# Kernel optimization log

Hardware: AMD Instinct MI355X
Metric: run time of the kernel (lower is better)

The kernel has to match this reference:

```python
import jax, jax.numpy as jnp
import numpy as np

B, T, I, H, S = 4096, 512, 4, 32, 4


def setup_inputs() -> dict:
    key = jax.random.key(0)
    ks = jax.random.split(key, 8)
    sc_ih = 1.0 / np.sqrt(H)
    return {
        "x": jax.random.normal(ks[0], (B, T, I), dtype=jnp.float32),
        "h0": jnp.zeros((1, B, H), dtype=jnp.float32),
        # PyTorch GRU params: weight_ih_l0 [3H, I] (r,z,n order), weight_hh_l0 [3H, H], biases [3H]
        "w_ih": jax.random.uniform(ks[1], (3 * H, I), jnp.float32, -sc_ih, sc_ih),
        "w_hh": jax.random.uniform(ks[2], (3 * H, H), jnp.float32, -sc_ih, sc_ih),
        "b_ih": jax.random.uniform(ks[3], (3 * H,), jnp.float32, -sc_ih, sc_ih),
        "b_hh": jax.random.uniform(ks[4], (3 * H,), jnp.float32, -sc_ih, sc_ih),
        "w_proj": jax.random.uniform(ks[5], (S, H), jnp.float32, -sc_ih, sc_ih),
        "b_proj": jax.random.uniform(ks[6], (S,), jnp.float32, -sc_ih, sc_ih),
    }


def _gru(x, h0, w_ih, w_hh, b_ih, b_hh):
    # Precompute input contributions for all timesteps: [B, T, 3H]
    xg = jnp.einsum('bti,gi->btg', x, w_ih) + b_ih
    xg_t = jnp.transpose(xg, (1, 0, 2))  # [T, B, 3H]
    h = h0[0]  # [B, H] (num_layers == 1)
    Hdim = w_hh.shape[1]

    def step(h, xg_step):
        hg = h @ w_hh.T + b_hh  # [B, 3H]
        xr, xz, xn = jnp.split(xg_step, 3, axis=-1)
        hr, hz, hn = jnp.split(hg, 3, axis=-1)
        r = jax.nn.sigmoid(xr + hr)
        z = jax.nn.sigmoid(xz + hz)
        n = jnp.tanh(xn + r * hn)
        h_new = (1.0 - z) * n + z * h
        return h_new, h_new

    hT, outs = jax.lax.scan(step, h, xg_t)
    out = jnp.transpose(outs, (1, 0, 2))  # [B, T, H]
    return out, hT[None]  # hn: [1, B, H]


def reference(x, h0, w_ih, w_hh, b_ih, b_hh, w_proj, b_proj):
    out, hn = _gru(x, h0, w_ih, w_hh, b_ih, b_hh)
    state = jnp.einsum('bth,sh->bts', out, w_proj) + b_proj  # [B, T, S]
    return state, hn
```

## Files before the change

### kernel.cpp

```cpp
#include <hip/hip_runtime.h>
#include <stdint.h>

#define BB 4096
#define TT 512
#define II 4
#define HH 32
#define SS 4

__device__ __forceinline__ float fast_sigm(float a) {
  return __builtin_amdgcn_rcpf(1.0f + __expf(-a));
}
__device__ __forceinline__ float fast_tanh(float y) {
  return 1.0f - 2.0f * __builtin_amdgcn_rcpf(__expf(2.0f * y) + 1.0f);
}

__global__ __launch_bounds__(256, 2) void gru_kernel(
    const float* __restrict__ x, const float* __restrict__ h0,
    const float* __restrict__ w_ih, const float* __restrict__ w_hh,
    const float* __restrict__ b_ih, const float* __restrict__ b_hh,
    const float* __restrict__ w_proj, const float* __restrict__ b_proj,
    float* __restrict__ out) {
  const int tid  = threadIdx.x;
  const int wid  = tid >> 6;
  const int lane = tid & 63;
  const int g    = lane >> 5;
  const int j    = lane & 31;
  const int row  = wid * 2 + g;
  const int b    = blockIdx.x * 8 + row;

  __shared__ float lds_h[8][36];
  float* lrow = &lds_h[row][0];

  const float4* whh4 = (const float4*)w_hh;
  float4 wr[8], wz[8], wn[8];
#pragma unroll
  for (int c = 0; c < 8; ++c) {
    wr[c] = whh4[(0 * HH + j) * 8 + c];
    wz[c] = whh4[(1 * HH + j) * 8 + c];
    wn[c] = whh4[(2 * HH + j) * 8 + c];
  }
  const float4* wih4 = (const float4*)w_ih;
  const float4 wir = wih4[0 * HH + j];
  const float4 wiz = wih4[1 * HH + j];
  const float4 win = wih4[2 * HH + j];
  const float bir = b_ih[0 * HH + j], biz = b_ih[1 * HH + j], bin_ = b_ih[2 * HH + j];
  const float bhr = b_hh[0 * HH + j], bhz = b_hh[1 * HH + j], bhn = b_hh[2 * HH + j];

  const int s_idx = j & 3;
  const int c_idx = j >> 2;
  const float4* wp4 = (const float4*)w_proj;
  const float4 wp = wp4[s_idx * 8 + c_idx];
  const float bp = b_proj[s_idx];

  float h_self = h0[(size_t)b * HH + j];
  lrow[j] = h_self;

  const float4* xp = (const float4*)(x + (size_t)b * TT * II);
  float* outp = out + (size_t)b * TT * SS;

  float4 xv = xp[0];

  for (int t = 0; t < TT; ++t) {
    float4 xvn = xp[(t + 1 < TT) ? (t + 1) : t];

    float4 ha[8];
#pragma unroll
    for (int c = 0; c < 8; ++c) ha[c] = *(const float4*)&lrow[c * 4];

    float xr = fmaf(wir.x, xv.x, fmaf(wir.y, xv.y, fmaf(wir.z, xv.z, fmaf(wir.w, xv.w, bir))));
    float xz = fmaf(wiz.x, xv.x, fmaf(wiz.y, xv.y, fmaf(wiz.z, xv.z, fmaf(wiz.w, xv.w, biz))));
    float xn = fmaf(win.x, xv.x, fmaf(win.y, xv.y, fmaf(win.z, xv.z, fmaf(win.w, xv.w, bin_))));

    float hr = bhr, hz = bhz, hn = bhn;
#pragma unroll
    for (int c = 0; c < 8; ++c) {
      hr = fmaf(wr[c].x, ha[c].x, hr); hr = fmaf(wr[c].y, ha[c].y, hr);
      hr = fmaf(wr[c].z, ha[c].z, hr); hr = fmaf(wr[c].w, ha[c].w, hr);
      hz = fmaf(wz[c].x, ha[c].x, hz); hz = fmaf(wz[c].y, ha[c].y, hz);
      hz = fmaf(wz[c].z, ha[c].z, hz); hz = fmaf(wz[c].w, ha[c].w, hz);
      hn = fmaf(wn[c].x, ha[c].x, hn); hn = fmaf(wn[c].y, ha[c].y, hn);
      hn = fmaf(wn[c].z, ha[c].z, hn); hn = fmaf(wn[c].w, ha[c].w, hn);
    }

    const float r  = fast_sigm(xr + hr);
    const float zz = fast_sigm(xz + hz);
    const float nn = fast_tanh(fmaf(r, hn, xn));
    const float hnew = fmaf(zz, h_self - nn, nn);
    h_self = hnew;

    lrow[j] = hnew;

    const float4 hc = *(const float4*)&lrow[c_idx * 4];
    float v = fmaf(wp.x, hc.x, fmaf(wp.y, hc.y, fmaf(wp.z, hc.z, wp.w * hc.w)));
    v += __shfl_xor(v, 4, 64);
    v += __shfl_xor(v, 8, 64);
    v += __shfl_xor(v, 16, 64);
    if (c_idx == 0) {
      outp[t * SS + s_idx] = v + bp;
    }

    xv = xvn;
  }

  out[(size_t)BB * TT * SS + (size_t)b * HH + j] = h_self;
}

extern "C" void kernel_launch(void* const* d_in, const int* in_sizes, int n_in,
                              void* d_out, int out_size, void* d_ws, size_t ws_size,
                              hipStream_t stream) {
  const float* x      = (const float*)d_in[0];
  const float* h0     = (const float*)d_in[1];
  const float* w_ih   = (const float*)d_in[2];
  const float* w_hh   = (const float*)d_in[3];
  const float* b_ih   = (const float*)d_in[4];
  const float* b_hh   = (const float*)d_in[5];
  const float* w_proj = (const float*)d_in[6];
  const float* b_proj = (const float*)d_in[7];
  float* out = (float*)d_out;

  dim3 grid(BB / 8), block(256);
  hipLaunchKernelGGL(gru_kernel, grid, block, 0, stream,
                     x, h0, w_ih, w_hh, b_ih, b_hh, w_proj, b_proj, out);
}
```

Measured before the change: 332.5 us.

## Split gate work across half-waves with packed fp16 weights and mixed FMA

Restructures the per-step GRU work so each half-wave computes two gate projections for both batch rows of the wave. Group 0 does r and z, and group 1 does n plus the output projection, which is folded in as an extra weight row. Partial sums are exchanged with a 32-lane shuffle. Weights are packed to fp16 in registers and used via v_fma_mix_f32, halving weight register count and removing the separate projection reduction shuffles. The projection is delayed by one step, which adds an extra loop iteration, and fp16 weights reduce accuracy.

```diff
diff --git a/kernel.cpp b/kernel.cpp
--- a/kernel.cpp
+++ b/kernel.cpp
@@ -3,7 +3,6 @@
 
 #define BB 4096
 #define TT 512
-#define II 4
 #define HH 32
 #define SS 4
 
@@ -14,95 +13,121 @@
   return 1.0f - 2.0f * __builtin_amdgcn_rcpf(__expf(2.0f * y) + 1.0f);
 }
 
-__global__ __launch_bounds__(256, 2) void gru_kernel(
-    const float* __restrict__ x, const float* __restrict__ h0,
-    const float* __restrict__ w_ih, const float* __restrict__ w_hh,
-    const float* __restrict__ b_ih, const float* __restrict__ b_hh,
-    const float* __restrict__ w_proj, const float* __restrict__ b_proj,
-    float* __restrict__ out) {
+#define PKH(dst, lo, hi)                                                       \
+  asm volatile("v_cvt_pkrtz_f16_f32 %0, %1, %2" : "=v"(dst) : "v"(lo), "v"(hi))
+#define MIXLO(acc, w, h)                                                       \
+  asm("v_fma_mix_f32 %0, %1, %2, %0 op_sel:[0,0,0] op_sel_hi:[1,0,0]"          \
+      : "+v"(acc) : "v"(w), "v"(h))
+#define MIXHI(acc, w, h)                                                       \
+  asm("v_fma_mix_f32 %0, %1, %2, %0 op_sel:[1,0,0] op_sel_hi:[1,0,0]"          \
+      : "+v"(acc) : "v"(w), "v"(h))
+#define MIXQ(acc, W, c, q)                                                     \
+  MIXLO(acc, W[2*(c)], (q).x); MIXHI(acc, W[2*(c)], (q).y);                    \
+  MIXLO(acc, W[2*(c)+1], (q).z); MIXHI(acc, W[2*(c)+1], (q).w)
+
+__global__ void __launch_bounds__(256, 2)
+gru_kernel(const float* __restrict__ x, const float* __restrict__ h0,
+           const float* __restrict__ w_ih, const float* __restrict__ w_hh,
+           const float* __restrict__ b_ih, const float* __restrict__ b_hh,
+           const float* __restrict__ w_proj, const float* __restrict__ b_proj,
+           float* __restrict__ out) {
   const int tid  = threadIdx.x;
   const int wid  = tid >> 6;
   const int lane = tid & 63;
-  const int g    = lane >> 5;
   const int j    = lane & 31;
-  const int row  = wid * 2 + g;
-  const int b    = blockIdx.x * 8 + row;
+  const int grp  = lane >> 5;
+  const int rowF = wid * 2 + grp;
+  const int bF   = blockIdx.x * 8 + rowF;
 
-  __shared__ float lds_h[8][36];
-  float* lrow = &lds_h[row][0];
+  __shared__ float hl[8][36];
+  float* lrowF = &hl[rowF][0];
+  const float4* lrowX = (const float4*)lrowF;
+  const float4* lrowY = (const float4*)&hl[wid * 2 + (1 - grp)][0];
 
-  const float4* whh4 = (const float4*)w_hh;
-  float4 wr[8], wz[8], wn[8];
-#pragma unroll
-  for (int c = 0; c < 8; ++c) {
-    wr[c] = whh4[(0 * HH + j) * 8 + c];
-    wz[c] = whh4[(1 * HH + j) * 8 + c];
-    wn[c] = whh4[(2 * HH + j) * 8 + c];
-  }
-  const float4* wih4 = (const float4*)w_ih;
-  const float4 wir = wih4[0 * HH + j];
-  const float4 wiz = wih4[1 * HH + j];
-  const float4 win = wih4[2 * HH + j];
-  const float bir = b_ih[0 * HH + j], biz = b_ih[1 * HH + j], bin_ = b_ih[2 * HH + j];
-  const float bhr = b_hh[0 * HH + j], bhz = b_hh[1 * HH + j], bhn = b_hh[2 * HH + j];
-
-  const int s_idx = j & 3;
-  const int c_idx = j >> 2;
-  const float4* wp4 = (const float4*)w_proj;
-  const float4 wp = wp4[s_idx * 8 + c_idx];
-  const float bp = b_proj[s_idx];
-
-  float h_self = h0[(size_t)b * HH + j];
-  lrow[j] = h_self;
-
-  const float4* xp = (const float4*)(x + (size_t)b * TT * II);
-  float* outp = out + (size_t)b * TT * SS;
-
-  float4 xv = xp[0];
-
-  for (int t = 0; t < TT; ++t) {
-    float4 xvn = xp[(t + 1 < TT) ? (t + 1) : t];
-
-    float4 ha[8];
-#pragma unroll
-    for (int c = 0; c < 8; ++c) ha[c] = *(const float4*)&lrow[c * 4];
-
-    float xr = fmaf(wir.x, xv.x, fmaf(wir.y, xv.y, fmaf(wir.z, xv.z, fmaf(wir.w, xv.w, bir))));
-    float xz = fmaf(wiz.x, xv.x, fmaf(wiz.y, xv.y, fmaf(wiz.z, xv.z, fmaf(wiz.w, xv.w, biz))));
-    float xn = fmaf(win.x, xv.x, fmaf(win.y, xv.y, fmaf(win.z, xv.z, fmaf(win.w, xv.w, bin_))));
-
-    float hr = bhr, hz = bhz, hn = bhn;
+  uint32_t W0[16], W1[16], XW0[2], XW1[2];
+  {
+    const float4* p0 = (const float4*)(grp ? (w_hh + (64 + j) * HH)
+                                           : (w_hh + j * HH));
+    const float4* p1 = (const float4*)(grp ? (w_proj + (j & 3) * HH)
+                                           : (w_hh + (32 + j) * HH));
 #pragma unroll
     for (int c = 0; c < 8; ++c) {
-      hr = fmaf(wr[c].x, ha[c].x, hr); hr = fmaf(wr[c].y, ha[c].y, hr);
-      hr = fmaf(wr[c].z, ha[c].z, hr); hr = fmaf(wr[c].w, ha[c].w, hr);
-      hz = fmaf(wz[c].x, ha[c].x, hz); hz = fmaf(wz[c].y, ha[c].y, hz);
-      hz = fmaf(wz[c].z, ha[c].z, hz); hz = fmaf(wz[c].w, ha[c].w, hz);
-      hn = fmaf(wn[c].x, ha[c].x, hn); hn = fmaf(wn[c].y, ha[c].y, hn);
-      hn = fmaf(wn[c].z, ha[c].z, hn); hn = fmaf(wn[c].w, ha[c].w, hn);
+      const float4 q0 = p0[c], q1 = p1[c];
+      PKH(W0[2*c], q0.x, q0.y); PKH(W0[2*c+1], q0.z, q0.w);
+      PKH(W1[2*c], q1.x, q1.y); PKH(W1[2*c+1], q1.z, q1.w);
+    }
+    const float4 qx0 = *(const float4*)(grp ? (w_ih + (64 + j) * 4)
+                                            : (w_ih + j * 4));
+    const float4 qx1 = *(const float4*)(grp ? (w_ih + (64 + j) * 4)
+                                            : (w_ih + (32 + j) * 4));
+    PKH(XW0[0], qx0.x, qx0.y); PKH(XW0[1], qx0.z, qx0.w);
+    PKH(XW1[0], qx1.x, qx1.y); PKH(XW1[1], qx1.z, qx1.w);
+  }
+
+  const float bx0 = grp ? b_ih[64 + j] : b_ih[j];
+  const float bx1 = grp ? 0.0f         : b_ih[32 + j];
+  const float bh0 = grp ? b_hh[64 + j] : b_hh[j];
+  const float bh1 = grp ? 0.0f         : b_hh[32 + j];
+  const float bp  = b_proj[j & 3];
+
+  float h_self = h0[(size_t)bF * HH + j];
+  lrowF[j] = h_self;
+
+  const float4* xF = (const float4*)(x + (size_t)bF * TT * 4);
+  const float4* xO = (const float4*)(x + (size_t)(bF ^ 1) * TT * 4);
+  float* outF = out + (size_t)bF * TT * SS;
+
+  for (int t = 0; t <= TT; ++t) {
+    const int tc = (t < TT) ? t : (TT - 1);
+    const float4 xvF = xF[tc];
+    const float4 xvO = xO[tc];
+
+    float4 hx[8], hy[8];
+#pragma unroll
+    for (int c = 0; c < 8; ++c) { hx[c] = lrowX[c]; hy[c] = lrowY[c]; }
+
+    float xa_x0 = bx0, xa_y0 = bx0, xa_x1 = bx1, xa_y1 = bx1;
+    MIXLO(xa_x0, XW0[0], xvF.x); MIXHI(xa_x0, XW0[0], xvF.y);
+    MIXLO(xa_x0, XW0[1], xvF.z); MIXHI(xa_x0, XW0[1], xvF.w);
+    MIXLO(xa_y0, XW0[0], xvO.x); MIXHI(xa_y0, XW0[0], xvO.y);
+    MIXLO(xa_y0, XW0[1], xvO.z); MIXHI(xa_y0, XW0[1], xvO.w);
+    MIXLO(xa_x1, XW1[0], xvF.x); MIXHI(xa_x1, XW1[0], xvF.y);
+    MIXLO(xa_x1, XW1[1], xvF.z); MIXHI(xa_x1, XW1[1], xvF.w);
+    MIXLO(xa_y1, XW1[0], xvO.x); MIXHI(xa_y1, XW1[0], xvO.y);
+    MIXLO(xa_y1, XW1[1], xvO.z); MIXHI(xa_y1, XW1[1], xvO.w);
+
+    float a_x0 = bh0, a_y0 = bh0, a_x1 = bh1, a_y1 = bh1;
+#pragma unroll
+    for (int c = 0; c < 8; ++c) {
+      MIXQ(a_x0, W0, c, hx[c]);
+      MIXQ(a_y0, W0, c, hy[c]);
+      MIXQ(a_x1, W1, c, hx[c]);
+      MIXQ(a_y1, W1, c, hy[c]);
     }
 
-    const float r  = fast_sigm(xr + hr);
-    const float zz = fast_sigm(xz + hz);
-    const float nn = fast_tanh(fmaf(r, hn, xn));
-    const float hnew = fmaf(zz, h_self - nn, nn);
+    const float e0 = __shfl_xor(a_y0, 32, 64);
+    const float e1 = __shfl_xor(xa_y0, 32, 64);
+    const float e2 = __shfl_xor(a_y1, 32, 64);
+    const float e3 = __shfl_xor(xa_y1, 32, 64);
+
+    const float rp = (grp ? e1 : xa_x0) + (grp ? e0 : a_x0);
+    const float zp = (grp ? e3 : xa_x1) + (grp ? e2 : a_x1);
+    const float nh = grp ? a_x0 : e0;
+    const float xn = grp ? xa_x0 : e1;
+    const float pv = grp ? a_x1 : e2;
+
+    if (t > 0 && j < 4) outF[(t - 1) * SS + j] = pv + bp;
+    if (t == TT) break;
+
+    const float r  = fast_sigm(rp);
+    const float z  = fast_sigm(zp);
+    const float n  = fast_tanh(fmaf(r, nh, xn));
+    const float hnew = fmaf(z, h_self - n, n);
     h_self = hnew;
-
-    lrow[j] = hnew;
-
-    const float4 hc = *(const float4*)&lrow[c_idx * 4];
-    float v = fmaf(wp.x, hc.x, fmaf(wp.y, hc.y, fmaf(wp.z, hc.z, wp.w * hc.w)));
-    v += __shfl_xor(v, 4, 64);
-    v += __shfl_xor(v, 8, 64);
-    v += __shfl_xor(v, 16, 64);
-    if (c_idx == 0) {
-      outp[t * SS + s_idx] = v + bp;
-    }
-
-    xv = xvn;
+    lrowF[j] = hnew;
   }
 
-  out[(size_t)BB * TT * SS + (size_t)b * HH + j] = h_self;
+  out[(size_t)BB * TT * SS + (size_t)bF * HH + j] = h_self;
 }
 
 extern "C" void kernel_launch(void* const* d_in, const int* in_sizes, int n_in,
```

After: 517.3 us. +55.6%, slower.
